# Performance work log

Measured on AMD Instinct MI355X. Metric: run time of the kernel, lower is better.

Reference implementation:

```python
import jax, jax.numpy as jnp
import numpy as np

B, T, D = 1, 2048, 4096
H, KV, HD = 32, 8, 128          # num_heads, num_kv_heads, head_dim
G = H // KV                     # kv groups
ROPE_THETA = 1000000.0
EPS = 1e-6


def _rmsnorm(x, w):
    # per-last-dim RMSNorm in fp32, as in Qwen3RMSNorm
    var = jnp.mean(jnp.square(x.astype(jnp.float32)), axis=-1, keepdims=True)
    return w * (x * jax.lax.rsqrt(var + EPS)).astype(x.dtype)


def _rotate_half(x):
    x1, x2 = x[..., : HD // 2], x[..., HD // 2 :]
    return jnp.concatenate([-x2, x1], axis=-1)


def setup_inputs() -> dict:
    key = jax.random.key(0)
    ks = jax.random.split(key, 7)
    s = 1.0 / np.sqrt(D)
    return {
        "hidden_states": jax.random.normal(ks[0], (B, T, D), dtype=jnp.float32),
        "Wq": jax.random.normal(ks[1], (D, H * HD), dtype=jnp.float32) * s,
        "Wk": jax.random.normal(ks[2], (D, KV * HD), dtype=jnp.float32) * s,
        "Wv": jax.random.normal(ks[3], (D, KV * HD), dtype=jnp.float32) * s,
        "Wo": jax.random.normal(ks[4], (H * HD, D), dtype=jnp.float32) * s,
        "q_norm_w": jnp.ones((HD,), dtype=jnp.float32),
        "k_norm_w": jnp.ones((HD,), dtype=jnp.float32),
    }


def reference(hidden_states, Wq, Wk, Wv, Wo, q_norm_w, k_norm_w):
    x = hidden_states
    # projections -> [B, heads, T, HD]
    q = (x @ Wq).reshape(B, T, H, HD).transpose(0, 2, 1, 3)
    k = (x @ Wk).reshape(B, T, KV, HD).transpose(0, 2, 1, 3)
    v = (x @ Wv).reshape(B, T, KV, HD).transpose(0, 2, 1, 3)

    # QK RMSNorm over head_dim
    q = _rmsnorm(q, q_norm_w)
    k = _rmsnorm(k, k_norm_w)

    # RoPE (self-attention path)
    inv_freq = 1.0 / (ROPE_THETA ** (jnp.arange(0, HD, 2, dtype=jnp.float32) / HD))
    freqs = jnp.arange(T, dtype=jnp.float32)[:, None] * inv_freq[None, :]  # [T, HD/2]
    emb = jnp.concatenate([freqs, freqs], axis=-1)                        # [T, HD]
    cos, sin = jnp.cos(emb)[None, None], jnp.sin(emb)[None, None]
    q = q * cos + _rotate_half(q) * sin
    k = k * cos + _rotate_half(k) * sin

    # GQA: group Q heads instead of repeat_interleaving K/V
    qg = q.reshape(B, KV, G, T, HD)  # head h attends kv head h // G
    scale = 1.0 / np.sqrt(HD)
    scores = jnp.einsum("bkgqd,bksd->bkgqs", qg, k) * scale  # [B,KV,G,Tq,Ts]

    causal = jnp.tril(jnp.ones((T, T), dtype=bool))
    scores = jnp.where(causal[None, None, None], scores, -jnp.inf)
    attn = jax.nn.softmax(scores, axis=-1)

    out = jnp.einsum("bkgqs,bksd->bkgqd", attn, v)            # [B,KV,G,T,HD]
    out = out.reshape(B, H, T, HD).transpose(0, 2, 1, 3).reshape(B, T, H * HD)
    return out @ Wo
```

## Files before the change

### kernel.cpp

```cpp
#include <hip/hip_runtime.h>
#include <math.h>

typedef __bf16 bf16;
typedef __bf16 bf16x8 __attribute__((ext_vector_type(8)));
typedef float f32x4 __attribute__((ext_vector_type(4)));

constexpr int cT = 2048;
constexpr int cD = 4096;
constexpr int cH = 32;
constexpr int cKV = 8;
constexpr int cHD = 128;
constexpr float SCALE = 0.08838834764831845f;

__device__ __forceinline__ void gl_lds16(const bf16* g, bf16* l) {
  __builtin_amdgcn_global_load_lds(
      (const __attribute__((address_space(1))) unsigned*)g,
      (__attribute__((address_space(3))) unsigned*)l, 16, 0, 0);
}

__device__ inline bf16x8 load8_cvt(const float* __restrict__ p) {
  float4 a = *(const float4*)p;
  float4 b = *(const float4*)(p + 4);
  bf16x8 r;
  r[0] = (bf16)a.x; r[1] = (bf16)a.y; r[2] = (bf16)a.z; r[3] = (bf16)a.w;
  r[4] = (bf16)b.x; r[5] = (bf16)b.y; r[6] = (bf16)b.z; r[7] = (bf16)b.w;
  return r;
}

__global__ __launch_bounds__(256) void convert_kernel(const float* __restrict__ s,
                                                      bf16* __restrict__ d) {
  const size_t i = (size_t)(blockIdx.x * 256 + threadIdx.x) * 8;
  *(bf16x8*)(d + i) = load8_cvt(s + i);
}

__global__ __launch_bounds__(256) void convT_kernel(const float* __restrict__ src,
                                                    bf16* __restrict__ dst,
                                                    int R, int C) {
  __shared__ float t[64][65];
  const int r0 = blockIdx.y * 64, c0 = blockIdx.x * 64;
  const int tid = threadIdx.x;
  {
    const int lr = tid >> 4, lc = (tid & 15) * 4;
#pragma unroll
    for (int i = 0; i < 4; ++i) {
      float4 v4 = *(const float4*)(src + (size_t)(r0 + lr + i * 16) * C + c0 + lc);
      t[lr + i * 16][lc] = v4.x;
      t[lr + i * 16][lc + 1] = v4.y;
      t[lr + i * 16][lc + 2] = v4.z;
      t[lr + i * 16][lc + 3] = v4.w;
    }
  }
  __syncthreads();
  {
    const int c = tid >> 2, rb = (tid & 3) * 16;
#pragma unroll
    for (int half = 0; half < 2; ++half) {
      bf16x8 o;
#pragma unroll
      for (int j = 0; j < 8; ++j) o[j] = (bf16)t[rb + half * 8 + j][c];
      *(bf16x8*)(dst + (size_t)(c0 + c) * R + r0 + rb + half * 8) = o;
    }
  }
}

template <int BN, typename OutT>
__global__ __launch_bounds__(256) void gemm_bt_kernel(const bf16* __restrict__ A,
                                                      const bf16* __restrict__ BT,
                                                      OutT* __restrict__ C,
                                                      int M, int N, int K) {
  __shared__ __align__(16) bf16 As[128][32];
  __shared__ __align__(16) bf16 Bs[BN][32];
  constexpr int TN = BN / 32;

  const int tid = threadIdx.x;
  const int lane = tid & 63, w = tid >> 6;
  const int ln = lane & 15, kg = lane >> 4;
  const int m0 = blockIdx.y * 128, n0 = blockIdx.x * BN;
  const int wm = (w >> 1) * 64;
  const int wn = (w & 1) * (BN / 2);

  f32x4 acc[4][TN] = {};

  const int srow = lane >> 2;
  const int schk = (lane & 3) * 8;
  const bf16* aG = A + (size_t)(m0 + srow) * K + schk;
  const bf16* bG = BT + (size_t)(n0 + srow) * K + schk;

  for (int kt = 0; kt < K; kt += 32) {
#pragma unroll
    for (int j = 0; j < 2; ++j)
      gl_lds16(aG + (size_t)(w * 32 + j * 16) * K + kt, &As[w * 32 + j * 16][0]);
#pragma unroll
    for (int j = 0; j < BN / 64; ++j)
      gl_lds16(bG + (size_t)(w * (BN / 4) + j * 16) * K + kt,
               &Bs[w * (BN / 4) + j * 16][0]);
    __syncthreads();

    bf16x8 af[4], bfr[TN];
#pragma unroll
    for (int tm = 0; tm < 4; ++tm)
      af[tm] = *(const bf16x8*)(&As[wm + tm * 16 + ln][kg * 8]);
#pragma unroll
    for (int tn = 0; tn < TN; ++tn)
      bfr[tn] = *(const bf16x8*)(&Bs[wn + tn * 16 + ln][kg * 8]);
#pragma unroll
    for (int tm = 0; tm < 4; ++tm)
#pragma unroll
      for (int tn = 0; tn < TN; ++tn)
        acc[tm][tn] = __builtin_amdgcn_mfma_f32_16x16x32_bf16(
            af[tm], bfr[tn], acc[tm][tn], 0, 0, 0);
    __syncthreads();
  }

#pragma unroll
  for (int tm = 0; tm < 4; ++tm)
#pragma unroll
    for (int tn = 0; tn < TN; ++tn)
#pragma unroll
      for (int r = 0; r < 4; ++r)
        C[(size_t)(m0 + wm + tm * 16 + kg * 4 + r) * N + n0 + wn + tn * 16 + ln] =
            (OutT)acc[tm][tn][r];
}

__global__ __launch_bounds__(256) void norm_rope_kernel(bf16* __restrict__ q,
                                                        bf16* __restrict__ kv,
                                                        const float* __restrict__ qw,
                                                        const float* __restrict__ kw) {
  const int gw = (blockIdx.x * 256 + threadIdx.x) >> 6;
  const int lane = threadIdx.x & 63;
  bf16* base;
  const float* wgt;
  float post;
  int t;
  if (gw < cT * cH) {
    t = gw >> 5;
    int h = gw & 31;
    base = q + (size_t)t * (cH * cHD) + h * cHD;
    wgt = qw;
    post = SCALE;
  } else {
    int g2 = gw - cT * cH;
    t = g2 >> 3;
    int h = g2 & 7;
    base = kv + (size_t)t * (2 * cKV * cHD) + h * cHD;
    wgt = kw;
    post = 1.0f;
  }
  const int d0 = lane * 2;
  float x0 = (float)base[d0], x1 = (float)base[d0 + 1];
  float ss = x0 * x0 + x1 * x1;
#pragma unroll
  for (int off = 32; off > 0; off >>= 1) ss += __shfl_xor(ss, off, 64);
  const float rs = rsqrtf(ss * (1.0f / 128.0f) + 1e-6f);
  float y0 = x0 * rs * wgt[d0];
  float y1 = x1 * rs * wgt[d0 + 1];
  float p0 = __shfl_xor(y0, 32, 64);
  float p1 = __shfl_xor(y1, 32, 64);
  const float sgn = (lane < 32) ? -1.0f : 1.0f;
  const int fi = d0 & 63;
  const float c1 = -19.93156856932417f / 64.0f;
  float inv0 = exp2f((float)fi * c1);
  float inv1 = exp2f((float)(fi + 1) * c1);
  float a0 = (float)t * inv0, a1 = (float)t * inv1;
  float o0 = (y0 * cosf(a0) + sgn * p0 * sinf(a0)) * post;
  float o1 = (y1 * cosf(a1) + sgn * p1 * sinf(a1)) * post;
  base[d0] = (bf16)o0;
  base[d0 + 1] = (bf16)o1;
}

__global__ void bound_kernel(const float* __restrict__ qw,
                             const float* __restrict__ kw,
                             float* __restrict__ cb) {
  const int lane = threadIdx.x;
  float mq = fmaxf(fabsf(qw[lane]), fabsf(qw[lane + 64]));
  float mk = fmaxf(fabsf(kw[lane]), fabsf(kw[lane + 64]));
#pragma unroll
  for (int off = 32; off > 0; off >>= 1) {
    mq = fmaxf(mq, __shfl_xor(mq, off, 64));
    mk = fmaxf(mk, __shfl_xor(mk, off, 64));
  }
  if (lane == 0) *cb = 128.0f * SCALE * mq * mk + 1e-3f;
}

__global__ __launch_bounds__(256) void flash_kernel(const bf16* __restrict__ q,
                                                    const bf16* __restrict__ kv,
                                                    const float* __restrict__ cb,
                                                    bf16* __restrict__ out) {
  __shared__ bf16 Ks[64][136];
  __shared__ bf16 VT[128][72];
  __shared__ bf16 Ps[4][32][72];

  constexpr int KVS = 2 * cKV * cHD;
  const int qt = (blockIdx.y < 16) ? (15 - blockIdx.x) : blockIdx.x;
  const int h = blockIdx.y;
  const int qm0 = qt * 128;
  const int kh = h >> 2;
  const int tid = threadIdx.x;
  const int lane = tid & 63, w = tid >> 6;
  const int ln = lane & 15, kg = lane >> 4;
  const float C = *cb;
  const int row0 = qm0 + w * 32;

  bf16x8 qa[2][4];
#pragma unroll
  for (int mt = 0; mt < 2; ++mt) {
    const bf16* qrow =
        q + (size_t)(row0 + mt * 16 + ln) * (cH * cHD) + h * cHD + kg * 8;
#pragma unroll
    for (int kk = 0; kk < 4; ++kk) qa[mt][kk] = *(const bf16x8*)(qrow + kk * 32);
  }

  const int sl = tid >> 2, sc = tid & 3;
  const int vp = tid & 31, vc = tid >> 5;
  const bf16* kbase = kv + (size_t)sl * KVS + kh * cHD + sc * 32;
  const bf16* vbase = kv + cKV * cHD + (size_t)(2 * vp) * KVS + kh * cHD + vc * 16;

  float l_r[2][4] = {};
  f32x4 o_acc[2][8] = {};

  const int nkt = 2 * qt + 2;

  bf16x8 kr[4], vr[4];
#pragma unroll
  for (int i = 0; i < 4; ++i) kr[i] = *(const bf16x8*)(kbase + i * 8);
  vr[0] = *(const bf16x8*)(vbase);
  vr[1] = *(const bf16x8*)(vbase + 8);
  vr[2] = *(const bf16x8*)(vbase + KVS);
  vr[3] = *(const bf16x8*)(vbase + KVS + 8);

  for (int kt = 0; kt < nkt; ++kt) {
#pragma unroll
    for (int i = 0; i < 4; ++i)
      *(bf16x8*)(&Ks[sl][sc * 32 + i * 8]) = kr[i];
#pragma unroll
    for (int i = 0; i < 8; ++i) {
      union { bf16 hh[2]; unsigned u; } pk;
      pk.hh[0] = vr[0][i]; pk.hh[1] = vr[2][i];
      *(unsigned*)(&VT[vc * 16 + i][2 * vp]) = pk.u;
      pk.hh[0] = vr[1][i]; pk.hh[1] = vr[3][i];
      *(unsigned*)(&VT[vc * 16 + 8 + i][2 * vp]) = pk.u;
    }
    __syncthreads();

    if (kt + 1 < nkt) {
      const bf16* kn = kbase + (size_t)(kt + 1) * 64 * KVS;
      const bf16* vn = vbase + (size_t)(kt + 1) * 64 * KVS;
#pragma unroll
      for (int i = 0; i < 4; ++i) kr[i] = *(const bf16x8*)(kn + i * 8);
      vr[0] = *(const bf16x8*)(vn);
      vr[1] = *(const bf16x8*)(vn + 8);
      vr[2] = *(const bf16x8*)(vn + KVS);
      vr[3] = *(const bf16x8*)(vn + KVS + 8);
    }

    f32x4 s_acc[2][4] = {};
    __builtin_amdgcn_s_setprio(1);
#pragma unroll
    for (int kk = 0; kk < 4; ++kk)
#pragma unroll
      for (int nt = 0; nt < 4; ++nt) {
        bf16x8 bfr = *(const bf16x8*)(&Ks[nt * 16 + ln][kk * 32 + kg * 8]);
        s_acc[0][nt] = __builtin_amdgcn_mfma_f32_16x16x32_bf16(
            qa[0][kk], bfr, s_acc[0][nt], 0, 0, 0);
        s_acc[1][nt] = __builtin_amdgcn_mfma_f32_16x16x32_bf16(
            qa[1][kk], bfr, s_acc[1][nt], 0, 0, 0);
      }
    __builtin_amdgcn_s_setprio(0);

    const bool edge = (kt * 64 + 63 > row0);
#pragma unroll
    for (int mt = 0; mt < 2; ++mt)
#pragma unroll
      for (int nt = 0; nt < 4; ++nt)
#pragma unroll
        for (int r = 0; r < 4; ++r) {
          float pe = __expf(s_acc[mt][nt][r] - C);
          if (edge) {
            int col = kt * 64 + nt * 16 + ln;
            int row = row0 + mt * 16 + kg * 4 + r;
            if (col > row) pe = 0.f;
          }
          l_r[mt][r] += pe;
          Ps[w][mt * 16 + kg * 4 + r][nt * 16 + ln] = (bf16)pe;
        }

    __builtin_amdgcn_s_setprio(1);
#pragma unroll
    for (int kk2 = 0; kk2 < 2; ++kk2) {
      bf16x8 pa0 = *(const bf16x8*)(&Ps[w][ln][kk2 * 32 + kg * 8]);
      bf16x8 pa1 = *(const bf16x8*)(&Ps[w][16 + ln][kk2 * 32 + kg * 8]);
#pragma unroll
      for (int dt = 0; dt < 8; ++dt) {
        bf16x8 vb = *(const bf16x8*)(&VT[dt * 16 + ln][kk2 * 32 + kg * 8]);
        o_acc[0][dt] = __builtin_amdgcn_mfma_f32_16x16x32_bf16(
            pa0, vb, o_acc[0][dt], 0, 0, 0);
        o_acc[1][dt] = __builtin_amdgcn_mfma_f32_16x16x32_bf16(
            pa1, vb, o_acc[1][dt], 0, 0, 0);
      }
    }
    __builtin_amdgcn_s_setprio(0);
    __syncthreads();
  }

#pragma unroll
  for (int mt = 0; mt < 2; ++mt)
#pragma unroll
    for (int r = 0; r < 4; ++r) {
      float l = l_r[mt][r];
#pragma unroll
      for (int off = 1; off <= 8; off <<= 1) l += __shfl_xor(l, off, 64);
      l_r[mt][r] = 1.0f / l;
    }

#pragma unroll
  for (int mt = 0; mt < 2; ++mt) {
    bf16* op = out + (size_t)(row0 + mt * 16 + kg * 4) * (cH * cHD) + h * cHD + ln;
#pragma unroll
    for (int dt = 0; dt < 8; ++dt)
#pragma unroll
      for (int r = 0; r < 4; ++r)
        op[(size_t)r * (cH * cHD) + dt * 16] = (bf16)(o_acc[mt][dt][r] * l_r[mt][r]);
  }
}

extern "C" void kernel_launch(void* const* d_in, const int* in_sizes, int n_in,
                              void* d_out, int out_size, void* d_ws, size_t ws_size,
                              hipStream_t stream) {
  const float* x  = (const float*)d_in[0];
  const float* Wq = (const float*)d_in[1];
  const float* Wk = (const float*)d_in[2];
  const float* Wv = (const float*)d_in[3];
  const float* Wo = (const float*)d_in[4];
  const float* qw = (const float*)d_in[5];
  const float* kw = (const float*)d_in[6];
  float* out = (float*)d_out;

  char* ws = (char*)d_ws;
  bf16* xb   = (bf16*)ws;
  bf16* WqT  = (bf16*)(ws + (16u << 20));
  bf16* WkvT = (bf16*)(ws + (16u << 20));
  bf16* kvb  = (bf16*)(ws + (32u << 20));
  float* cb  = (float*)(ws + (46u << 20));
  bf16* qb   = (bf16*)(ws + (48u << 20));
  bf16* attn = (bf16*)ws;
  bf16* WoT  = (bf16*)(ws + (16u << 20));

  convert_kernel<<<(cT * cD) / (8 * 256), 256, 0, stream>>>(x, xb);
  convT_kernel<<<dim3(cD / 64, cD / 64), 256, 0, stream>>>(Wq, WqT, cD, cD);
  gemm_bt_kernel<128, bf16><<<dim3(cD / 128, cT / 128), 256, 0, stream>>>(
      xb, WqT, qb, cT, cD, cD);
  convT_kernel<<<dim3((cKV * cHD) / 64, cD / 64), 256, 0, stream>>>(Wk, WkvT, cD, cKV * cHD);
  convT_kernel<<<dim3((cKV * cHD) / 64, cD / 64), 256, 0, stream>>>(
      Wv, WkvT + (size_t)(cKV * cHD) * cD, cD, cKV * cHD);
  gemm_bt_kernel<64, bf16><<<dim3((2 * cKV * cHD) / 64, cT / 128), 256, 0, stream>>>(
      xb, WkvT, kvb, cT, 2 * cKV * cHD, cD);
  norm_rope_kernel<<<(cT * (cH + cKV)) / 4, 256, 0, stream>>>(qb, kvb, qw, kw);
  bound_kernel<<<1, 64, 0, stream>>>(qw, kw, cb);
  flash_kernel<<<dim3(cT / 128, cH), 256, 0, stream>>>(qb, kvb, cb, attn);
  convT_kernel<<<dim3(cD / 64, cD / 64), 256, 0, stream>>>(Wo, WoT, cD, cD);
  gemm_bt_kernel<128, float><<<dim3(cD / 128, cT / 128), 256, 0, stream>>>(
      attn, WoT, out, cT, cD, cD);
}
```

Before: 595.1 us.

## Multi-stage LDS pipeline for bf16 GEMM with explicit vmcnt waits

```diff
diff --git a/kernel.cpp b/kernel.cpp
--- a/kernel.cpp
+++ b/kernel.cpp
@@ -16,6 +16,16 @@
   __builtin_amdgcn_global_load_lds(
       (const __attribute__((address_space(1))) unsigned*)g,
       (__attribute__((address_space(3))) unsigned*)l, 16, 0, 0);
+}
+
+template <int N>
+__device__ __forceinline__ void wait_vmcnt() {
+  if constexpr (N == 0) asm volatile("s_waitcnt vmcnt(0)" ::: "memory");
+  else if constexpr (N == 3) asm volatile("s_waitcnt vmcnt(3)" ::: "memory");
+  else if constexpr (N == 4) asm volatile("s_waitcnt vmcnt(4)" ::: "memory");
+  else if constexpr (N == 6) asm volatile("s_waitcnt vmcnt(6)" ::: "memory");
+  else if constexpr (N == 8) asm volatile("s_waitcnt vmcnt(8)" ::: "memory");
+  else static_assert(N == 0, "unsupported vmcnt literal");
 }
 
 __device__ inline bf16x8 load8_cvt(const float* __restrict__ p) {
@@ -68,9 +78,10 @@
                                                       const bf16* __restrict__ BT,
                                                       OutT* __restrict__ C,
                                                       int M, int N, int K) {
-  __shared__ __align__(16) bf16 As[128][32];
-  __shared__ __align__(16) bf16 Bs[BN][32];
+  __shared__ __align__(16) bf16 As[4][128][32];
+  __shared__ __align__(16) bf16 Bs[4][BN][32];
   constexpr int TN = BN / 32;
+  constexpr int LPS = 2 + BN / 64;
 
   const int tid = threadIdx.x;
   const int lane = tid & 63, w = tid >> 6;
@@ -86,31 +97,56 @@
   const bf16* aG = A + (size_t)(m0 + srow) * K + schk;
   const bf16* bG = BT + (size_t)(n0 + srow) * K + schk;
 
-  for (int kt = 0; kt < K; kt += 32) {
+  auto stage = [&](int slice) {
+    const int sb = slice & 3;
+    const int kt = slice * 32;
 #pragma unroll
     for (int j = 0; j < 2; ++j)
-      gl_lds16(aG + (size_t)(w * 32 + j * 16) * K + kt, &As[w * 32 + j * 16][0]);
+      gl_lds16(aG + (size_t)(w * 32 + j * 16) * K + kt, &As[sb][w * 32 + j * 16][0]);
 #pragma unroll
     for (int j = 0; j < BN / 64; ++j)
       gl_lds16(bG + (size_t)(w * (BN / 4) + j * 16) * K + kt,
-               &Bs[w * (BN / 4) + j * 16][0]);
-    __syncthreads();
-
+               &Bs[sb][w * (BN / 4) + j * 16][0]);
+  };
+
+  auto compute = [&](int slice) {
+    const int sb = slice & 3;
     bf16x8 af[4], bfr[TN];
 #pragma unroll
     for (int tm = 0; tm < 4; ++tm)
-      af[tm] = *(const bf16x8*)(&As[wm + tm * 16 + ln][kg * 8]);
+      af[tm] = *(const bf16x8*)(&As[sb][wm + tm * 16 + ln][kg * 8]);
 #pragma unroll
     for (int tn = 0; tn < TN; ++tn)
-      bfr[tn] = *(const bf16x8*)(&Bs[wn + tn * 16 + ln][kg * 8]);
+      bfr[tn] = *(const bf16x8*)(&Bs[sb][wn + tn * 16 + ln][kg * 8]);
 #pragma unroll
     for (int tm = 0; tm < 4; ++tm)
 #pragma unroll
       for (int tn = 0; tn < TN; ++tn)
         acc[tm][tn] = __builtin_amdgcn_mfma_f32_16x16x32_bf16(
             af[tm], bfr[tn], acc[tm][tn], 0, 0, 0);
-    __syncthreads();
-  }
+  };
+
+  const int NS = K / 32;
+
+  stage(0);
+  stage(1);
+  stage(2);
+
+  for (int s = 0; s < NS - 3; ++s) {
+    wait_vmcnt<2 * LPS>();
+    __builtin_amdgcn_s_barrier();
+    stage(s + 3);
+    compute(s);
+  }
+  wait_vmcnt<2 * LPS>();
+  __builtin_amdgcn_s_barrier();
+  compute(NS - 3);
+  wait_vmcnt<LPS>();
+  __builtin_amdgcn_s_barrier();
+  compute(NS - 2);
+  wait_vmcnt<0>();
+  __builtin_amdgcn_s_barrier();
+  compute(NS - 1);
 
 #pragma unroll
   for (int tm = 0; tm < 4; ++tm)
```

Result: no change. 600.6 us (+0.9%).
